# Kernel optimization log

Hardware: AMD Instinct MI355X
Metric: run time of the kernel (lower is better)

The kernel has to match this reference:

```python
import jax, jax.numpy as jnp
import numpy as np

N_NODES = 50000
N_EDGES = 600000
D = 128
PROP_STEPS = 4


def setup_inputs() -> dict:
    key = jax.random.key(0)
    ks = jax.random.split(key, 9)
    d = D
    inp = {
        "nodes_ft": jax.random.normal(ks[0], (N_NODES, d), dtype=jnp.float32),
        "adj_list": jax.random.randint(ks[1], (2, N_EDGES), 0, N_NODES, dtype=jnp.int32),
        # nodes_adj_state_bias, xavier-normal style scale
        "bias": jax.random.normal(ks[2], (1, d), dtype=jnp.float32) * (2.0 / (1 + d)) ** 0.5,
        # gate Linears: weight [2d, d] (x @ W + b convention), xavier-ish scale
        "Wr": jax.random.normal(ks[3], (2 * d, d), dtype=jnp.float32) * (1.0 / (2 * d)) ** 0.5,
        "br": jnp.zeros((d,), dtype=jnp.float32),
        "Wz": jax.random.normal(ks[4], (2 * d, d), dtype=jnp.float32) * (1.0 / (2 * d)) ** 0.5,
        "bz": jnp.zeros((d,), dtype=jnp.float32),
        "Wt": jax.random.normal(ks[5], (2 * d, d), dtype=jnp.float32) * (1.0 / (2 * d)) ** 0.5,
        "bt": jnp.zeros((d,), dtype=jnp.float32),
    }
    return inp


def reference(nodes_ft, adj_list, bias, Wr, br, Wz, bz, Wt, bt):
    n = nodes_ft.shape[0]
    dst, src = adj_list[0], adj_list[1]
    prior_h = nodes_ft
    h = prior_h
    # Faithful to source: prior_h is NOT updated inside the loop (original code bug),
    # so each step recomputes the same h.
    for _ in range(PROP_STEPS):
        msg = prior_h[src]                                   # [E, d] gather
        agg = jax.ops.segment_sum(msg, dst, num_segments=n)  # [N, d] scatter-add
        s = jax.nn.softmax(agg + bias, axis=-1)              # [N, d]
        tmp = jnp.concatenate([s, prior_h], axis=-1)          # [N, 2d]
        r = jax.nn.sigmoid(tmp @ Wr + br)
        z = jax.nn.sigmoid(tmp @ Wz + bz)
        h_hat = jnp.tanh(jnp.concatenate([s, r * prior_h], axis=-1) @ Wt + bt)
        h = (1.0 - z) * prior_h + z * h_hat
    return h
```

## Files before the change

kernel.cpp:

```cpp
#include <hip/hip_runtime.h>

#define NN 50000
#define NE 600000
#define DD 128
#define CAP 64

typedef __attribute__((ext_vector_type(8))) short s16x8;
typedef __attribute__((ext_vector_type(4))) float f32x4;

#define CNT_BYTES   (256 * 1024)
#define SLOT_OFF    CNT_BYTES
#define SLOT_BYTES  ((size_t)NN * CAP * 2)
#define WPACK_OFF   (SLOT_OFF + SLOT_BYTES)
#define WPACK_N     (3 * 8 * 8 * 512)
#define WPACK_BYTES ((size_t)WPACK_N * 2)
#define NBF_OFF     (WPACK_OFF + WPACK_BYTES)

#define FILL_BLOCKS ((NE + 255) / 256)
#define CONV_BLOCKS (WPACK_N / 256)
#define NBF_BLOCKS  ((NN * DD / 8) / 256)

__device__ __forceinline__ unsigned short f2bf(float f) {
    unsigned int u = __float_as_uint(f);
    unsigned int r = (u + 0x7fffu + ((u >> 16) & 1u)) >> 16;
    return (unsigned short)r;
}
__device__ __forceinline__ float bf2f(unsigned short h) {
    return __uint_as_float(((unsigned int)h) << 16);
}
__device__ __forceinline__ void accum8(float* x, uint4 v, float msk) {
    x[0] = fmaf(__uint_as_float(v.x << 16),          msk, x[0]);
    x[1] = fmaf(__uint_as_float(v.x & 0xffff0000u),  msk, x[1]);
    x[2] = fmaf(__uint_as_float(v.y << 16),          msk, x[2]);
    x[3] = fmaf(__uint_as_float(v.y & 0xffff0000u),  msk, x[3]);
    x[4] = fmaf(__uint_as_float(v.z << 16),          msk, x[4]);
    x[5] = fmaf(__uint_as_float(v.z & 0xffff0000u),  msk, x[5]);
    x[6] = fmaf(__uint_as_float(v.w << 16),          msk, x[6]);
    x[7] = fmaf(__uint_as_float(v.w & 0xffff0000u),  msk, x[7]);
}

__global__ __launch_bounds__(256) void prep_k(
    const int* __restrict__ adj, int* __restrict__ cnt, unsigned short* __restrict__ slots,
    const float* __restrict__ Wr, const float* __restrict__ Wz,
    const float* __restrict__ Wt, unsigned short* __restrict__ wp,
    const float* __restrict__ nodes, unsigned short* __restrict__ nbf)
{
    int b = blockIdx.x;
    if (b < FILL_BLOCKS) {
        int e = b * 256 + threadIdx.x;
        if (e >= NE) return;
        int d = adj[e];
        int pos = atomicAdd(&cnt[d], 1);
        if (pos < CAP) slots[(size_t)d * CAP + pos] = (unsigned short)adj[NE + e];
    } else if (b < FILL_BLOCKS + CONV_BLOCKS) {
        int t = (b - FILL_BLOCKS) * 256 + threadIdx.x;
        int j  = t & 7;
        int l  = (t >> 3) & 63;
        int kt = (t >> 9) & 7;
        int ct = (t >> 12) & 7;
        int g  = t >> 15;
        int k   = kt * 32 + ((l >> 4) & 3) * 8 + j;
        int col = ct * 16 + (l & 15);
        const float* W = (g == 0) ? Wr : (g == 1) ? Wz : Wt;
        wp[t] = f2bf(W[k * DD + col]);
    } else {
        int t = (b - FILL_BLOCKS - CONV_BLOCKS) * 256 + threadIdx.x;
        const float4* s4 = (const float4*)nodes + (size_t)t * 2;
        float4 a = s4[0], c4 = s4[1];
        uint4 o;
        o.x = (unsigned)f2bf(a.x)  | ((unsigned)f2bf(a.y)  << 16);
        o.y = (unsigned)f2bf(a.z)  | ((unsigned)f2bf(a.w)  << 16);
        o.z = (unsigned)f2bf(c4.x) | ((unsigned)f2bf(c4.y) << 16);
        o.w = (unsigned)f2bf(c4.z) | ((unsigned)f2bf(c4.w) << 16);
        ((uint4*)nbf)[t] = o;
    }
}

__global__ __launch_bounds__(256) void fused_k(
    const unsigned short* __restrict__ nbf,
    const int* __restrict__ adj,
    const int* __restrict__ cnt,
    const unsigned short* __restrict__ slots,
    const unsigned short* __restrict__ wp,
    const float* __restrict__ bias,
    const float* __restrict__ br, const float* __restrict__ bz, const float* __restrict__ bt,
    float* __restrict__ out)
{
    __shared__ unsigned short X[64][264];
    __shared__ unsigned short PH[64][128];
    const int tid  = threadIdx.x;
    const int w    = tid >> 6;
    const int l    = tid & 63;
    const int row0 = blockIdx.x * 64;
    const int q    = l >> 4;
    const int li   = l & 15;

    {
        const float4 bb0 = *(const float4*)(bias + 8 * li);
        const float4 bb1 = *(const float4*)(bias + 8 * li + 4);
        int rown = row0 + w * 16 + li;
        int c_all = cnt[rown < NN ? rown : 0];
        for (int j = 0; j < 16; ++j) {
            int lr   = w * 16 + j;
            int grow = row0 + lr;
            int gc   = grow < NN ? grow : 0;
            int c    = __shfl(c_all, j);
            uint4 phv = *(const uint4*)(nbf + (size_t)gc * DD + 8 * li);
            float x[8];
#pragma unroll
            for (int i = 0; i < 8; ++i) x[i] = 0.f;
            if (c <= CAP) {
                int myslot = (l < c) ? (int)slots[(size_t)gc * CAP + l] : 0;
                {
                    uint4 v[4]; float msk[4];
#pragma unroll
                    for (int i = 0; i < 4; ++i) {
                        int sp = i * 4 + q;
                        int s0 = __shfl(myslot, sp);
                        v[i] = *(const uint4*)(nbf + (size_t)s0 * DD + 8 * li);
                        msk[i] = (sp < c) ? 1.f : 0.f;
                    }
#pragma unroll
                    for (int i = 0; i < 4; ++i) accum8(x, v[i], msk[i]);
                }
                for (int jj = 16; jj < c; jj += 16) {
                    uint4 v[4]; float msk[4];
#pragma unroll
                    for (int i = 0; i < 4; ++i) {
                        int sp = jj + i * 4 + q;
                        int s0 = __shfl(myslot, sp & 63);
                        v[i] = *(const uint4*)(nbf + (size_t)s0 * DD + 8 * li);
                        msk[i] = (sp < c) ? 1.f : 0.f;
                    }
#pragma unroll
                    for (int i = 0; i < 4; ++i) accum8(x, v[i], msk[i]);
                }
            } else {
                int mi = 0;
                for (int base = 0; base < NE; base += 64) {
                    int e  = base + l;
                    int d  = (e < NE) ? adj[e] : -1;
                    int sv = (e < NE) ? adj[NE + e] : 0;
                    unsigned long long m = __ballot(d == grow);
                    while (m) {
                        int bpos = __ffsll((unsigned long long)m) - 1;
                        m &= m - 1;
                        int s0 = __shfl(sv, bpos);
                        if ((mi & 3) == q) {
                            uint4 v = *(const uint4*)(nbf + (size_t)s0 * DD + 8 * li);
                            accum8(x, v, 1.f);
                        }
                        ++mi;
                    }
                }
            }
#pragma unroll
            for (int i = 0; i < 8; ++i) {
                x[i] += __shfl_xor(x[i], 16);
                x[i] += __shfl_xor(x[i], 32);
            }
            x[0] += bb0.x; x[1] += bb0.y; x[2] += bb0.z; x[3] += bb0.w;
            x[4] += bb1.x; x[5] += bb1.y; x[6] += bb1.z; x[7] += bb1.w;
            float mx = x[0];
#pragma unroll
            for (int i = 1; i < 8; ++i) mx = fmaxf(mx, x[i]);
#pragma unroll
            for (int o = 1; o < 16; o <<= 1) mx = fmaxf(mx, __shfl_xor(mx, o));
            float e8[8], sm = 0.f;
#pragma unroll
            for (int i = 0; i < 8; ++i) { e8[i] = __expf(x[i] - mx); sm += e8[i]; }
#pragma unroll
            for (int o = 1; o < 16; o <<= 1) sm += __shfl_xor(sm, o);
            float inv = 1.f / sm;
            if (q == 0) {
                uint4 u;
                u.x = (unsigned)f2bf(e8[0] * inv) | ((unsigned)f2bf(e8[1] * inv) << 16);
                u.y = (unsigned)f2bf(e8[2] * inv) | ((unsigned)f2bf(e8[3] * inv) << 16);
                u.z = (unsigned)f2bf(e8[4] * inv) | ((unsigned)f2bf(e8[5] * inv) << 16);
                u.w = (unsigned)f2bf(e8[6] * inv) | ((unsigned)f2bf(e8[7] * inv) << 16);
                *(uint4*)&X[lr][8 * li] = u;
            } else if (q == 1) {
                *(uint4*)&X[lr][128 + 8 * li] = phv;
            } else if (q == 2) {
                *(uint4*)&PH[lr][8 * li] = phv;
            }
        }
    }

    const int rbase  = w * 16;
    const int mrow   = l & 15;
    const int quad   = l >> 4;
    const int col_in = l & 15;
    const int rq     = l >> 4;

    s16x8 a[8];
#pragma unroll
    for (int kt = 0; kt < 8; ++kt)
        a[kt] = *(const s16x8*)&X[rbase + mrow][kt * 32 + quad * 8];

    const s16x8* wp8 = (const s16x8*)wp;
    float zv[8][4];

#pragma unroll
    for (int ct = 0; ct < 8; ++ct) {
        int c = ct * 16 + col_in;
        float brv = br[c], bzv = bz[c];
        f32x4 ar = {brv, brv, brv, brv};
        f32x4 az = {bzv, bzv, bzv, bzv};
#pragma unroll
        for (int kt = 0; kt < 8; ++kt) {
            s16x8 bfr = wp8[((0 * 8 + ct) * 8 + kt) * 64 + l];
            s16x8 bfz = wp8[((1 * 8 + ct) * 8 + kt) * 64 + l];
            ar = __builtin_amdgcn_mfma_f32_16x16x32_bf16(a[kt], bfr, ar, 0, 0, 0);
            az = __builtin_amdgcn_mfma_f32_16x16x32_bf16(a[kt], bfz, az, 0, 0, 0);
        }
#pragma unroll
        for (int i = 0; i < 4; ++i) {
            float rr = 1.f / (1.f + __expf(-ar[i]));
            zv[ct][i] = 1.f / (1.f + __expf(-az[i]));
            int lr = rbase + rq * 4 + i;
            float ph = bf2f(X[lr][128 + c]);
            X[lr][128 + c] = f2bf(rr * ph);
        }
    }

#pragma unroll
    for (int kt = 4; kt < 8; ++kt)
        a[kt] = *(const s16x8*)&X[rbase + mrow][kt * 32 + quad * 8];

#pragma unroll
    for (int ct = 0; ct < 8; ++ct) {
        int c = ct * 16 + col_in;
        float btv = bt[c];
        f32x4 at = {btv, btv, btv, btv};
#pragma unroll
        for (int kt = 0; kt < 8; ++kt) {
            s16x8 bft = wp8[((2 * 8 + ct) * 8 + kt) * 64 + l];
            at = __builtin_amdgcn_mfma_f32_16x16x32_bf16(a[kt], bft, at, 0, 0, 0);
        }
#pragma unroll
        for (int i = 0; i < 4; ++i) {
            int lr   = rbase + rq * 4 + i;
            int grow = row0 + lr;
            if (grow < NN) {
                float hh = tanhf(at[i]);
                float z  = zv[ct][i];
                float ph = bf2f(PH[lr][c]);
                out[(size_t)grow * DD + c] = (1.f - z) * ph + z * hh;
            }
        }
    }
}

extern "C" void kernel_launch(void* const* d_in, const int* in_sizes, int n_in,
                              void* d_out, int out_size, void* d_ws, size_t ws_size,
                              hipStream_t stream) {
    const float* nodes = (const float*)d_in[0];
    const int*   adj   = (const int*)d_in[1];
    const float* bias  = (const float*)d_in[2];
    const float* Wr    = (const float*)d_in[3];
    const float* br    = (const float*)d_in[4];
    const float* Wz    = (const float*)d_in[5];
    const float* bz    = (const float*)d_in[6];
    const float* Wt    = (const float*)d_in[7];
    const float* bt    = (const float*)d_in[8];
    float* out = (float*)d_out;

    char* ws = (char*)d_ws;
    int*            cnt   = (int*)ws;
    unsigned short* slots = (unsigned short*)(ws + SLOT_OFF);
    unsigned short* wpack = (unsigned short*)(ws + WPACK_OFF);
    unsigned short* nbf   = (unsigned short*)(ws + NBF_OFF);

    hipMemsetAsync(cnt, 0, (size_t)NN * sizeof(int), stream);

    prep_k<<<FILL_BLOCKS + CONV_BLOCKS + NBF_BLOCKS, 256, 0, stream>>>(
        adj, cnt, slots, Wr, Wz, Wt, wpack, nodes, nbf);
    fused_k<<<(NN + 63) / 64, 256, 0, stream>>>(nbf, adj, cnt, slots, wpack,
                                                bias, br, bz, bt, out);
}
```

Before: 244.6 us.

## Prefetch next row's neighbor gathers and reuse shared memory for the residual state

The aggregation loop is software-pipelined. While one row's gathered messages are being accumulated and its softmax computed, the slot list, count, prior state and first 16 neighbor rows for the next row are already being loaded, and slot indices are fetched two rows ahead. This aims to hide global gather latency. The separate PH shared array is removed: r*h is written into the now-consumed softmax columns of X, so the prior state stays in place for the final blend. Shared memory drops, launch bounds now request higher occupancy, and the edge-fill prep handles two edges per thread with vector loads. The cost is more live registers, which risks spills under the tighter occupancy bound.

New measurement: 205.2 us. 1.19x faster.

```diff
diff --git a/kernel.cpp b/kernel.cpp
--- a/kernel.cpp
+++ b/kernel.cpp
@@ -16,7 +16,7 @@
 #define WPACK_BYTES ((size_t)WPACK_N * 2)
 #define NBF_OFF     (WPACK_OFF + WPACK_BYTES)
 
-#define FILL_BLOCKS ((NE + 255) / 256)
+#define FILL_BLOCKS ((NE / 2 + 255) / 256)
 #define CONV_BLOCKS (WPACK_N / 256)
 #define NBF_BLOCKS  ((NN * DD / 8) / 256)
 
@@ -47,11 +47,14 @@
 {
     int b = blockIdx.x;
     if (b < FILL_BLOCKS) {
-        int e = b * 256 + threadIdx.x;
-        if (e >= NE) return;
-        int d = adj[e];
-        int pos = atomicAdd(&cnt[d], 1);
-        if (pos < CAP) slots[(size_t)d * CAP + pos] = (unsigned short)adj[NE + e];
+        int t = b * 256 + threadIdx.x;
+        if (2 * t >= NE) return;
+        int2 d2 = *(const int2*)(adj + 2 * t);
+        int2 s2 = *(const int2*)(adj + NE + 2 * t);
+        int p0 = atomicAdd(&cnt[d2.x], 1);
+        if (p0 < CAP) slots[(size_t)d2.x * CAP + p0] = (unsigned short)s2.x;
+        int p1 = atomicAdd(&cnt[d2.y], 1);
+        if (p1 < CAP) slots[(size_t)d2.y * CAP + p1] = (unsigned short)s2.y;
     } else if (b < FILL_BLOCKS + CONV_BLOCKS) {
         int t = (b - FILL_BLOCKS) * 256 + threadIdx.x;
         int j  = t & 7;
@@ -76,7 +79,7 @@
     }
 }
 
-__global__ __launch_bounds__(256) void fused_k(
+__global__ __launch_bounds__(256, 4) void fused_k(
     const unsigned short* __restrict__ nbf,
     const int* __restrict__ adj,
     const int* __restrict__ cnt,
@@ -87,7 +90,6 @@
     float* __restrict__ out)
 {
     __shared__ unsigned short X[64][264];
-    __shared__ unsigned short PH[64][128];
     const int tid  = threadIdx.x;
     const int w    = tid >> 6;
     const int l    = tid & 63;
@@ -98,37 +100,70 @@
     {
         const float4 bb0 = *(const float4*)(bias + 8 * li);
         const float4 bb1 = *(const float4*)(bias + 8 * li + 4);
-        int rown = row0 + w * 16 + li;
+        int rown  = row0 + (w << 4) + li;
         int c_all = cnt[rown < NN ? rown : 0];
+
+        unsigned short sraw[2];
+        uint4 vg[2][4]; float mg[2][4];
+        uint4 phg[2];
+        int   slotm[2], cj[2];
+
+        {
+            int g0 = row0 + (w << 4);
+            int gc0 = g0 < NN ? g0 : 0;
+            int gc1 = (g0 + 1) < NN ? (g0 + 1) : 0;
+            sraw[0] = slots[(size_t)gc0 * CAP + l];
+            sraw[1] = slots[(size_t)gc1 * CAP + l];
+            cj[0] = __shfl(c_all, 0);
+            slotm[0] = (l < cj[0]) ? (int)sraw[0] : 0;
+            if (q == 1) phg[0] = *(const uint4*)(nbf + (size_t)gc0 * DD + 8 * li);
+#pragma unroll
+            for (int i = 0; i < 4; ++i) {
+                int sp = i * 4 + q;
+                int s0 = __shfl(slotm[0], sp);
+                vg[0][i] = *(const uint4*)(nbf + (size_t)s0 * DD + 8 * li);
+                mg[0][i] = (sp < cj[0]) ? 1.f : 0.f;
+            }
+        }
+
+#pragma unroll
         for (int j = 0; j < 16; ++j) {
-            int lr   = w * 16 + j;
+            const int p = j & 1, pn = p ^ 1;
+            unsigned short snew = 0;
+            if (j + 2 < 16) {
+                int g2 = row0 + (w << 4) + j + 2;
+                int gc2 = g2 < NN ? g2 : 0;
+                snew = slots[(size_t)gc2 * CAP + l];
+            }
+            if (j + 1 < 16) {
+                int g1 = row0 + (w << 4) + j + 1;
+                int gc1 = g1 < NN ? g1 : 0;
+                cj[pn] = __shfl(c_all, j + 1);
+                slotm[pn] = (l < cj[pn]) ? (int)sraw[pn] : 0;
+                if (q == 1) phg[pn] = *(const uint4*)(nbf + (size_t)gc1 * DD + 8 * li);
+#pragma unroll
+                for (int i = 0; i < 4; ++i) {
+                    int sp = i * 4 + q;
+                    int s0 = __shfl(slotm[pn], sp);
+                    vg[pn][i] = *(const uint4*)(nbf + (size_t)s0 * DD + 8 * li);
+                    mg[pn][i] = (sp < cj[pn]) ? 1.f : 0.f;
+                }
+            }
+            int lr   = (w << 4) + j;
             int grow = row0 + lr;
-            int gc   = grow < NN ? grow : 0;
-            int c    = __shfl(c_all, j);
-            uint4 phv = *(const uint4*)(nbf + (size_t)gc * DD + 8 * li);
+            int c    = cj[p];
             float x[8];
 #pragma unroll
             for (int i = 0; i < 8; ++i) x[i] = 0.f;
             if (c <= CAP) {
-                int myslot = (l < c) ? (int)slots[(size_t)gc * CAP + l] : 0;
-                {
-                    uint4 v[4]; float msk[4];
-#pragma unroll
-                    for (int i = 0; i < 4; ++i) {
-                        int sp = i * 4 + q;
-                        int s0 = __shfl(myslot, sp);
-                        v[i] = *(const uint4*)(nbf + (size_t)s0 * DD + 8 * li);
-                        msk[i] = (sp < c) ? 1.f : 0.f;
-                    }
-#pragma unroll
-                    for (int i = 0; i < 4; ++i) accum8(x, v[i], msk[i]);
-                }
+#pragma unroll
+                for (int i = 0; i < 4; ++i) accum8(x, vg[p][i], mg[p][i]);
                 for (int jj = 16; jj < c; jj += 16) {
                     uint4 v[4]; float msk[4];
 #pragma unroll
                     for (int i = 0; i < 4; ++i) {
                         int sp = jj + i * 4 + q;
-                        int s0 = __shfl(myslot, sp & 63);
+                        int s0 = __shfl(slotm[p], sp & 63);
                         v[i] = *(const uint4*)(nbf + (size_t)s0 * DD + 8 * li);
                         msk[i] = (sp < c) ? 1.f : 0.f;
                     }
@@ -180,10 +215,9 @@
                 u.w = (unsigned)f2bf(e8[6] * inv) | ((unsigned)f2bf(e8[7] * inv) << 16);
                 *(uint4*)&X[lr][8 * li] = u;
             } else if (q == 1) {
-                *(uint4*)&X[lr][128 + 8 * li] = phv;
-            } else if (q == 2) {
-                *(uint4*)&PH[lr][8 * li] = phv;
-            }
+                *(uint4*)&X[lr][128 + 8 * li] = phg[p];
+            }
+            sraw[p] = snew;
         }
     }
 
@@ -220,13 +254,13 @@
             zv[ct][i] = 1.f / (1.f + __expf(-az[i]));
             int lr = rbase + rq * 4 + i;
             float ph = bf2f(X[lr][128 + c]);
-            X[lr][128 + c] = f2bf(rr * ph);
+            X[lr][c] = f2bf(rr * ph);
         }
     }
 
 #pragma unroll
     for (int kt = 4; kt < 8; ++kt)
-        a[kt] = *(const s16x8*)&X[rbase + mrow][kt * 32 + quad * 8];
+        a[kt] = *(const s16x8*)&X[rbase + mrow][(kt - 4) * 32 + quad * 8];
 
 #pragma unroll
     for (int ct = 0; ct < 8; ++ct) {
@@ -245,7 +279,7 @@
             if (grow < NN) {
                 float hh = tanhf(at[i]);
                 float z  = zv[ct][i];
-                float ph = bf2f(PH[lr][c]);
+                float ph = bf2f(X[lr][128 + c]);
                 out[(size_t)grow * DD + c] = (1.f - z) * ph + z * hh;
             }
         }
```
